# Performance work log

Measured on AMD Instinct MI355X. Metric: run time of the kernel, lower is better.

Reference implementation:

```python
import jax, jax.numpy as jnp
import numpy as np

V, BS, L, H, D = 32000, 2048, 6, 12, 768
B, T = 2, 2048
HD = D // H  # 64
STD = 0.02


def _ln(x, w, b):
    m = x.mean(-1, keepdims=True)
    v = x.var(-1, keepdims=True)
    return (x - m) / jnp.sqrt(v + 1e-5) * w + b


def setup_inputs() -> dict:
    key = jax.random.key(0)
    ks = jax.random.split(key, 7)
    idx = jax.random.randint(ks[0], (B, T), 0, V)
    tok_emb = jax.random.normal(ks[1], (V, D), jnp.float32) * STD   # tied with lm_head
    pos_emb = jax.random.normal(ks[2], (BS, D), jnp.float32) * STD
    qkv_w = jax.random.normal(ks[3], (L, D, 3 * D), jnp.float32) * STD
    out_w = jax.random.normal(ks[4], (L, D, D), jnp.float32) * STD
    ff1_w = jax.random.normal(ks[5], (L, D, 4 * D), jnp.float32) * STD
    ff2_w = jax.random.normal(ks[6], (L, 4 * D, D), jnp.float32) * STD
    ln1_w = jnp.ones((L, D)); ln1_b = jnp.zeros((L, D))
    ln2_w = jnp.ones((L, D)); ln2_b = jnp.zeros((L, D))
    lnf_w = jnp.ones((D,));  lnf_b = jnp.zeros((D,))
    return dict(idx=idx, tok_emb=tok_emb, pos_emb=pos_emb,
                ln1_w=ln1_w, ln1_b=ln1_b, qkv_w=qkv_w, out_w=out_w,
                ln2_w=ln2_w, ln2_b=ln2_b, ff1_w=ff1_w, ff2_w=ff2_w,
                lnf_w=lnf_w, lnf_b=lnf_b)


def reference(idx, tok_emb, pos_emb, ln1_w, ln1_b, qkv_w, out_w,
              ln2_w, ln2_b, ff1_w, ff2_w, lnf_w, lnf_b):
    Bb, Tt = idx.shape
    x = tok_emb[idx] + pos_emb[:Tt]          # [B,T,D]
    mask = jnp.tril(jnp.ones((Tt, Tt), bool))  # causal
    scale = jnp.asarray(np.sqrt(HD), x.dtype)

    def layer(x, p):
        l1w, l1b, Wqkv, Wout, l2w, l2b, W1, W2 = p
        h = _ln(x, l1w, l1b)
        q, k, v = jnp.split(h @ Wqkv, 3, axis=-1)
        hd = lambda t: t.reshape(Bb, Tt, H, HD).transpose(0, 2, 1, 3)  # [B,H,T,hd]
        q, k, v = hd(q), hd(k), hd(v)
        att = jnp.einsum('bhqd,bhkd->bhqk', q, k) / scale
        att = jnp.where(mask, att, -jnp.inf)
        att = jax.nn.softmax(att, axis=-1)
        y = jnp.einsum('bhqk,bhkd->bhqd', att, v)
        y = y.transpose(0, 2, 1, 3).reshape(Bb, Tt, D)
        x = x + y @ Wout
        h2 = _ln(x, l2w, l2b)
        x = x + jax.nn.gelu(h2 @ W1, approximate=False) @ W2
        return x, None

    x, _ = jax.lax.scan(layer, x, (ln1_w, ln1_b, qkv_w, out_w, ln2_w, ln2_b, ff1_w, ff2_w))
    x = _ln(x, lnf_w, lnf_b)
    return x @ tok_emb.T  # tied lm_head -> [B,T,V]
```

## Files before the change

### kernel.cpp

```cpp
#include <hip/hip_runtime.h>
#include <hip/hip_bf16.h>
#include <math.h>

typedef short short8 __attribute__((ext_vector_type(8)));
typedef short short4v __attribute__((ext_vector_type(4)));
typedef float f32x4 __attribute__((ext_vector_type(4)));
typedef unsigned short ushort_t;
typedef unsigned int uint_t;

#define D_MODEL 768
#define L_LAYERS 6
#define N_TOK 4096
#define T_SEQ 2048
#define H_HEADS 12
#define V_VOCAB 32000
#define L2E 1.44269504088896340736f

__device__ __forceinline__ ushort_t f2b(float f) {
  uint_t u = __builtin_bit_cast(uint_t, f);
  u += 0x7fffu + ((u >> 16) & 1u);
  return (ushort_t)(u >> 16);
}

__device__ __forceinline__ void gload_lds16(const void* g, void* l) {
  __builtin_amdgcn_global_load_lds(
      (const __attribute__((address_space(1))) unsigned int*)g,
      (__attribute__((address_space(3))) unsigned int*)l, 16, 0, 0);
}

__global__ void embed_kernel(const int* __restrict__ idx, const float* __restrict__ tok,
                             const float* __restrict__ pos, float* __restrict__ x) {
  int n = blockIdx.x;
  int tok_id = idx[n];
  int t = n & (T_SEQ - 1);
  const float* tr = tok + (size_t)tok_id * D_MODEL;
  const float* pr = pos + (size_t)t * D_MODEL;
  float* xr = x + (size_t)n * D_MODEL;
  for (int k = threadIdx.x; k < D_MODEL; k += 256) xr[k] = tr[k] + pr[k];
}

__global__ void ln_kernel(const float* __restrict__ x, const float* __restrict__ w,
                          const float* __restrict__ b, ushort_t* __restrict__ out) {
  int r = blockIdx.x, tid = threadIdx.x;
  const float* xr = x + (size_t)r * D_MODEL;
  float v0 = xr[tid], v1 = xr[tid + 256], v2 = xr[tid + 512];
  __shared__ float red[8];
  int l = tid & 63, wv = tid >> 6;
  float s = v0 + v1 + v2;
#pragma unroll
  for (int m = 32; m >= 1; m >>= 1) s += __shfl_xor(s, m, 64);
  if (l == 0) red[wv] = s;
  __syncthreads();
  float mean = (red[0] + red[1] + red[2] + red[3]) * (1.f / 768.f);
  float t0 = v0 - mean, t1 = v1 - mean, t2 = v2 - mean;
  float sq = t0 * t0 + t1 * t1 + t2 * t2;
#pragma unroll
  for (int m = 32; m >= 1; m >>= 1) sq += __shfl_xor(sq, m, 64);
  if (l == 0) red[4 + wv] = sq;
  __syncthreads();
  float var = (red[4] + red[5] + red[6] + red[7]) * (1.f / 768.f);
  float rstd = rsqrtf(var + 1e-5f);
  ushort_t* orow = out + (size_t)r * D_MODEL;
  orow[tid]       = f2b(t0 * rstd * w[tid] + b[tid]);
  orow[tid + 256] = f2b(t1 * rstd * w[tid + 256] + b[tid + 256]);
  orow[tid + 512] = f2b(t2 * rstd * w[tid + 512] + b[tid + 512]);
}

__global__ void transpose_cast_kernel(const float* __restrict__ in, ushort_t* __restrict__ out,
                                      int R, int C) {
  __shared__ float tile[32][33];
  size_t zoff = (size_t)blockIdx.z * R * C;
  in += zoff; out += zoff;
  int c0 = blockIdx.x * 32, r0 = blockIdx.y * 32;
  int tx = threadIdx.x, ty = threadIdx.y;
#pragma unroll
  for (int i = 0; i < 4; i++)
    tile[ty + i * 8][tx] = in[(size_t)(r0 + ty + i * 8) * C + (c0 + tx)];
  __syncthreads();
#pragma unroll
  for (int i = 0; i < 4; i++)
    out[(size_t)(c0 + ty + i * 8) * R + (r0 + tx)] = f2b(tile[tx][ty + i * 8]);
}

__global__ void cast_kernel(const float* __restrict__ in, ushort_t* __restrict__ out, int n) {
  for (int i = blockIdx.x * 256 + threadIdx.x; i < n; i += gridDim.x * 256)
    out[i] = f2b(in[i]);
}

#define EPI_STORE 0
#define EPI_ADD 1
#define EPI_GELU 2
#define EPI_CASTB 3

template <int EPI>
__global__ __launch_bounds__(256) void gemm_nt(const ushort_t* __restrict__ A,
                                               const ushort_t* __restrict__ B,
                                               float* __restrict__ Cf,
                                               ushort_t* __restrict__ Cb,
                                               int M, int N, int K) {
  __shared__ __align__(16) ushort_t As[128 * 32];
  __shared__ __align__(16) ushort_t Bs[128 * 32];
  int t = threadIdx.x;
  int l = t & 63, wv = t >> 6;
  int wm = (wv >> 1) * 64, wn = (wv & 1) * 64;

  int nwg = gridDim.x * gridDim.y;
  int bid = blockIdx.y * gridDim.x + blockIdx.x;
  int qn = nwg >> 3, r8 = nwg & 7;
  int xcd = bid & 7, pos = bid >> 3;
  int wg = (xcd < r8 ? xcd * (qn + 1) : r8 * (qn + 1) + (xcd - r8) * qn) + pos;
  int bn = wg % gridDim.x, bm = wg / gridDim.x;

  int fr = l & 15, fq = l >> 4;

  int srow = t >> 2;
  int scol = (t & 3) * 8;
  const ushort_t* gA = A + (size_t)(bm * 128 + srow) * K + scol;
  const ushort_t* gB = B + (size_t)(bn * 128 + srow) * K + scol;
  ushort_t* lA0 = &As[(wv * 16) * 32];
  ushort_t* lA1 = &As[(64 + wv * 16) * 32];
  ushort_t* lB0 = &Bs[(wv * 16) * 32];
  ushort_t* lB1 = &Bs[(64 + wv * 16) * 32];

  f32x4 acc[4][4];
#pragma unroll
  for (int i = 0; i < 4; i++)
#pragma unroll
    for (int j = 0; j < 4; j++) acc[i][j] = (f32x4){0.f, 0.f, 0.f, 0.f};

  for (int kt = 0; kt < K; kt += 32) {
    gload_lds16(gA + kt, lA0);
    gload_lds16(gA + (size_t)64 * K + kt, lA1);
    gload_lds16(gB + kt, lB0);
    gload_lds16(gB + (size_t)64 * K + kt, lB1);
    __syncthreads();
    short8 af[4], bf[4];
#pragma unroll
    for (int i = 0; i < 4; i++)
      af[i] = *(const short8*)&As[(wm + i * 16 + fr) * 32 + fq * 8];
#pragma unroll
    for (int j = 0; j < 4; j++)
      bf[j] = *(const short8*)&Bs[(wn + j * 16 + fr) * 32 + fq * 8];
#pragma unroll
    for (int i = 0; i < 4; i++)
#pragma unroll
      for (int j = 0; j < 4; j++)
        acc[i][j] = __builtin_amdgcn_mfma_f32_16x16x32_bf16(af[i], bf[j], acc[i][j], 0, 0, 0);
    __syncthreads();
  }

  int row0 = bm * 128 + wm + fq * 4;
  int col0 = bn * 128 + wn + fr;
#pragma unroll
  for (int i = 0; i < 4; i++) {
#pragma unroll
    for (int j = 0; j < 4; j++) {
#pragma unroll
      for (int r = 0; r < 4; r++) {
        int row = row0 + i * 16 + r;
        int col = col0 + j * 16;
        size_t off = (size_t)row * N + col;
        float v = acc[i][j][r];
        if (EPI == EPI_STORE) {
          Cf[off] = v;
        } else if (EPI == EPI_ADD) {
          Cf[off] += v;
        } else if (EPI == EPI_GELU) {
          Cb[off] = f2b(0.5f * v * (1.f + erff(v * 0.70710678118f)));
        } else {
          Cb[off] = f2b(v);
        }
      }
    }
  }
}

__global__ __launch_bounds__(256) void attn_mfma(const ushort_t* __restrict__ qkv,
                                                 ushort_t* __restrict__ y) {
  __shared__ __align__(16) ushort_t Ks[64 * 64];
  __shared__ __align__(16) ushort_t Vt[64 * 64];

  int id = blockIdx.x;
  int bh = id % 24;
  int qb = 31 - id / 24;
  int b = bh / H_HEADS, h = bh % H_HEADS;
  int t = threadIdx.x, l = t & 63, w = t >> 6;
  int ql = l & 15, kg = l >> 4;
  int q0 = qb * 64;
  size_t base = (size_t)b * T_SEQ * 2304;
  int qrow = q0 + w * 16 + ql;

  const ushort_t* qptr = qkv + base + (size_t)qrow * 2304 + h * 64 + kg * 8;
  short8 qf0 = *(const short8*)qptr;
  short8 qf1 = *(const short8*)(qptr + 32);

  float mrun = -INFINITY, lrun = 0.f;
  f32x4 o[4];
#pragma unroll
  for (int jd = 0; jd < 4; jd++) o[jd] = (f32x4){0.f, 0.f, 0.f, 0.f};

  const ushort_t* kbase = qkv + base + 768 + h * 64;
  const ushort_t* vbase = qkv + base + 1536 + h * 64;

  for (int kt = 0; kt <= q0; kt += 64) {
#pragma unroll
    for (int i = 0; i < 2; i++) {
      int c = i * 256 + t;
      int key = c >> 3, dc = c & 7;
      short8 k8 = *(const short8*)(kbase + (size_t)(kt + key) * 2304 + dc * 8);
      *(short8*)&Ks[key * 64 + ((dc ^ (key & 7)) * 8)] = k8;
      int vd0 = dc * 8;
      short8 v8 = *(const short8*)(vbase + (size_t)(kt + key) * 2304 + vd0);
#pragma unroll
      for (int e = 0; e < 8; e++) {
        int d = vd0 + e;
        Vt[d * 64 + (((key >> 3) ^ (d & 7)) * 8) + (key & 7)] = (ushort_t)v8[e];
      }
    }
    __syncthreads();

    f32x4 s[4];
#pragma unroll
    for (int kb = 0; kb < 4; kb++) {
      s[kb] = (f32x4){0.f, 0.f, 0.f, 0.f};
      short8 kfa = *(const short8*)&Ks[(kb * 16 + ql) * 64 + ((kg ^ (ql & 7)) * 8)];
      s[kb] = __builtin_amdgcn_mfma_f32_16x16x32_bf16(kfa, qf0, s[kb], 0, 0, 0);
      short8 kfb = *(const short8*)&Ks[(kb * 16 + ql) * 64 + (((kg + 4) ^ (ql & 7)) * 8)];
      s[kb] = __builtin_amdgcn_mfma_f32_16x16x32_bf16(kfb, qf1, s[kb], 0, 0, 0);
    }
#pragma unroll
    for (int kb = 0; kb < 4; kb++)
#pragma unroll
      for (int r = 0; r < 4; r++) s[kb][r] *= 0.125f;

    if (kt == q0) {
      int qloc = w * 16 + ql;
#pragma unroll
      for (int kb = 0; kb < 4; kb++)
#pragma unroll
        for (int r = 0; r < 4; r++) {
          int keyloc = kb * 16 + kg * 4 + r;
          if (keyloc > qloc) s[kb][r] = -INFINITY;
        }
    }

    float pm = -INFINITY;
#pragma unroll
    for (int kb = 0; kb < 4; kb++)
#pragma unroll
      for (int r = 0; r < 4; r++) pm = fmaxf(pm, s[kb][r]);
    pm = fmaxf(pm, __shfl_xor(pm, 16, 64));
    pm = fmaxf(pm, __shfl_xor(pm, 32, 64));
    float mnew = fmaxf(mrun, pm);
    float ps = 0.f;
#pragma unroll
    for (int kb = 0; kb < 4; kb++)
#pragma unroll
      for (int r = 0; r < 4; r++) {
        float p = exp2f((s[kb][r] - mnew) * L2E);
        s[kb][r] = p;
        ps += p;
      }
    ps += __shfl_xor(ps, 16, 64);
    ps += __shfl_xor(ps, 32, 64);
    float alpha = exp2f((mrun - mnew) * L2E);
    lrun = lrun * alpha + ps;
    mrun = mnew;
#pragma unroll
    for (int jd = 0; jd < 4; jd++)
#pragma unroll
      for (int r = 0; r < 4; r++) o[jd][r] *= alpha;

#pragma unroll
    for (int h2 = 0; h2 < 2; h2++) {
      short8 pb;
#pragma unroll
      for (int e = 0; e < 8; e++) {
        int r = e & 3, eb = e >> 2;
        int src = ql + 16 * (2 * (kg & 1) + eb);
        float vA = __shfl(s[2 * h2][r], src, 64);
        float vB = __shfl(s[2 * h2 + 1][r], src, 64);
        float v = (kg >> 1) ? vB : vA;
        pb[e] = (short)f2b(v);
      }
#pragma unroll
      for (int jd = 0; jd < 4; jd++) {
        short8 vf = *(const short8*)&Vt[(jd * 16 + ql) * 64 + (((kg + 4 * h2) ^ (ql & 7)) * 8)];
        o[jd] = __builtin_amdgcn_mfma_f32_16x16x32_bf16(vf, pb, o[jd], 0, 0, 0);
      }
    }
    __syncthreads();
  }

  float inv = 1.f / lrun;
  size_t yb = (size_t)(b * T_SEQ + qrow) * D_MODEL + h * 64;
#pragma unroll
  for (int jd = 0; jd < 4; jd++) {
    short4v pk;
#pragma unroll
    for (int r = 0; r < 4; r++) pk[r] = (short)f2b(o[jd][r] * inv);
    *(short4v*)&y[yb + jd * 16 + kg * 4] = pk;
  }
}

extern "C" void kernel_launch(void* const* d_in, const int* in_sizes, int n_in,
                              void* d_out, int out_size, void* d_ws, size_t ws_size,
                              hipStream_t stream) {
  const int*   idx     = (const int*)d_in[0];
  const float* tok_emb = (const float*)d_in[1];
  const float* pos_emb = (const float*)d_in[2];
  const float* ln1_w   = (const float*)d_in[3];
  const float* ln1_b   = (const float*)d_in[4];
  const float* qkv_w   = (const float*)d_in[5];
  const float* out_w   = (const float*)d_in[6];
  const float* ln2_w   = (const float*)d_in[7];
  const float* ln2_b   = (const float*)d_in[8];
  const float* ff1_w   = (const float*)d_in[9];
  const float* ff2_w   = (const float*)d_in[10];
  const float* lnf_w   = (const float*)d_in[11];
  const float* lnf_b   = (const float*)d_in[12];
  float* out = (float*)d_out;

  char* ws = (char*)d_ws;
  ushort_t* WqkvT = (ushort_t*)ws; ws += (size_t)L_LAYERS * 2304 * 768 * 2;
  ushort_t* WoutT = (ushort_t*)ws; ws += (size_t)L_LAYERS * 768 * 768 * 2;
  ushort_t* W1T   = (ushort_t*)ws; ws += (size_t)L_LAYERS * 3072 * 768 * 2;
  ushort_t* W2T   = (ushort_t*)ws; ws += (size_t)L_LAYERS * 768 * 3072 * 2;
  ushort_t* EmbB  = (ushort_t*)ws; ws += (size_t)V_VOCAB * 768 * 2;
  float*    x     = (float*)ws;    ws += (size_t)N_TOK * 768 * 4;
  ushort_t* hbuf  = (ushort_t*)ws; ws += (size_t)N_TOK * 768 * 2;
  ushort_t* qkvb  = (ushort_t*)ws; ws += (size_t)N_TOK * 2304 * 2;
  ushort_t* ybuf  = (ushort_t*)ws; ws += (size_t)N_TOK * 768 * 2;
  ushort_t* abuf  = (ushort_t*)ws; ws += (size_t)N_TOK * 3072 * 2;

  dim3 tb(32, 8);
  transpose_cast_kernel<<<dim3(2304 / 32, 768 / 32, 6), tb, 0, stream>>>(qkv_w, WqkvT, 768, 2304);
  transpose_cast_kernel<<<dim3(768 / 32, 768 / 32, 6), tb, 0, stream>>>(out_w, WoutT, 768, 768);
  transpose_cast_kernel<<<dim3(3072 / 32, 768 / 32, 6), tb, 0, stream>>>(ff1_w, W1T, 768, 3072);
  transpose_cast_kernel<<<dim3(768 / 32, 3072 / 32, 6), tb, 0, stream>>>(ff2_w, W2T, 3072, 768);
  cast_kernel<<<12000, 256, 0, stream>>>(tok_emb, EmbB, V_VOCAB * 768);
  embed_kernel<<<N_TOK, 256, 0, stream>>>(idx, tok_emb, pos_emb, x);

  for (int layer = 0; layer < L_LAYERS; layer++) {
    ln_kernel<<<N_TOK, 256, 0, stream>>>(x, ln1_w + layer * 768, ln1_b + layer * 768, hbuf);
    gemm_nt<EPI_CASTB><<<dim3(2304 / 128, N_TOK / 128), 256, 0, stream>>>(
        hbuf, WqkvT + (size_t)layer * 2304 * 768, nullptr, qkvb, N_TOK, 2304, 768);
    attn_mfma<<<24 * 32, 256, 0, stream>>>(qkvb, ybuf);
    gemm_nt<EPI_ADD><<<dim3(768 / 128, N_TOK / 128), 256, 0, stream>>>(
        ybuf, WoutT + (size_t)layer * 768 * 768, x, nullptr, N_TOK, 768, 768);
    ln_kernel<<<N_TOK, 256, 0, stream>>>(x, ln2_w + layer * 768, ln2_b + layer * 768, hbuf);
    gemm_nt<EPI_GELU><<<dim3(3072 / 128, N_TOK / 128), 256, 0, stream>>>(
        hbuf, W1T + (size_t)layer * 3072 * 768, nullptr, abuf, N_TOK, 3072, 768);
    gemm_nt<EPI_ADD><<<dim3(768 / 128, N_TOK / 128), 256, 0, stream>>>(
        abuf, W2T + (size_t)layer * 768 * 3072, x, nullptr, N_TOK, 768, 3072);
  }
  ln_kernel<<<N_TOK, 256, 0, stream>>>(x, lnf_w, lnf_b, hbuf);
  gemm_nt<EPI_STORE><<<dim3(V_VOCAB / 128, N_TOK / 128), 256, 0, stream>>>(
      hbuf, EmbB, out, nullptr, N_TOK, V_VOCAB, 768);
}
```

Before: 2.660 ms.

## Add triple-buffered 256-row GEMM with XCD-aware tile mapping for large GEMMs

Introduces a new 512-thread GEMM kernel with 256xBN tiles, a three-stage LDS ring buffer fed by direct global-to-LDS loads, XOR-swizzled LDS layout, and s_setprio around the MFMA blocks. Workgroup IDs are remapped so consecutive tiles land on the same XCD, for better L2 reuse. The QKV, FF1 and LM-head GEMMs use it, aiming to hide global load latency behind MFMA work and raise per-block reuse. Larger tiles mean fewer blocks for the smaller GEMMs, and the hand-placed waitcnt/barrier scheme depends on an exact count of loads in flight.

```diff
diff --git a/kernel.cpp b/kernel.cpp
--- a/kernel.cpp
+++ b/kernel.cpp
@@ -153,6 +153,144 @@
   int col0 = bn * 128 + wn + fr;
 #pragma unroll
   for (int i = 0; i < 4; i++) {
+#pragma unroll
+    for (int j = 0; j < 4; j++) {
+#pragma unroll
+      for (int r = 0; r < 4; r++) {
+        int row = row0 + i * 16 + r;
+        int col = col0 + j * 16;
+        size_t off = (size_t)row * N + col;
+        float v = acc[i][j][r];
+        if (EPI == EPI_STORE) {
+          Cf[off] = v;
+        } else if (EPI == EPI_ADD) {
+          Cf[off] += v;
+        } else if (EPI == EPI_GELU) {
+          Cb[off] = f2b(0.5f * v * (1.f + erff(v * 0.70710678118f)));
+        } else {
+          Cb[off] = f2b(v);
+        }
+      }
+    }
+  }
+}
+
+template <int BN, int EPI>
+__global__ __launch_bounds__(512) void gemm_nt_pipe(const ushort_t* __restrict__ A,
+                                                    const ushort_t* __restrict__ B,
+                                                    float* __restrict__ Cf,
+                                                    ushort_t* __restrict__ Cb,
+                                                    int M, int N, int K) {
+  constexpr int WGM = (BN == 256) ? 2 : 4;
+  constexpr int WGN = 8 / WGM;
+  constexpr int WTM = 256 / WGM;
+  constexpr int NI = WTM / 16;
+  constexpr int NLB = (BN == 256) ? 2 : 1;
+  __shared__ __align__(16) ushort_t As[3][256 * 32];
+  __shared__ __align__(16) ushort_t Bs[3][BN * 32];
+
+  int t = threadIdx.x, l = t & 63, wid = t >> 6;
+  int fr = l & 15, fq = l >> 4;
+  int wm_g = wid / WGN, wn_g = wid % WGN;
+  int RM = wm_g * WTM, CN = wn_g * 64;
+
+  int nbm = M >> 8;
+  int nwg = gridDim.x;
+  int bid = blockIdx.x;
+  int q8 = nwg >> 3, r8 = nwg & 7;
+  int xcd = bid & 7, pos = bid >> 3;
+  int wg = (xcd < r8 ? xcd * (q8 + 1) : r8 * (q8 + 1) + (xcd - r8) * q8) + pos;
+  int bm = wg % nbm, bn = wg / nbm;
+
+  int rlow = l >> 2;
+  int rowA0 = (wid * 2) * 16 + rlow;
+  int rowA1 = (wid * 2 + 1) * 16 + rlow;
+  const ushort_t* gA0 = A + (size_t)(bm * 256 + rowA0) * K + (((l & 3) ^ ((rowA0 >> 1) & 3)) * 8);
+  const ushort_t* gA1 = A + (size_t)(bm * 256 + rowA1) * K + (((l & 3) ^ ((rowA1 >> 1) & 3)) * 8);
+  int rowB0 = (wid * NLB) * 16 + rlow;
+  int rowB1 = (wid * NLB + 1) * 16 + rlow;
+  const ushort_t* gB0 = B + (size_t)(bn * BN + rowB0) * K + (((l & 3) ^ ((rowB0 >> 1) & 3)) * 8);
+  const ushort_t* gB1 = B + (size_t)(bn * BN + rowB1) * K + (((l & 3) ^ ((rowB1 >> 1) & 3)) * 8);
+
+  f32x4 acc[NI][4];
+#pragma unroll
+  for (int i = 0; i < NI; i++)
+#pragma unroll
+    for (int j = 0; j < 4; j++) acc[i][j] = (f32x4){0.f, 0.f, 0.f, 0.f};
+
+  int nt = K >> 5;
+
+#pragma unroll
+  for (int s = 0; s < 2; s++) {
+    gload_lds16(gA0 + s * 32, &As[s][(wid * 2) * 512]);
+    gload_lds16(gA1 + s * 32, &As[s][(wid * 2 + 1) * 512]);
+    gload_lds16(gB0 + s * 32, &Bs[s][(wid * NLB) * 512]);
+    if constexpr (NLB == 2) gload_lds16(gB1 + s * 32, &Bs[s][(wid * 2 + 1) * 512]);
+  }
+  if constexpr (NLB == 2) asm volatile("s_waitcnt vmcnt(4)" ::: "memory");
+  else                    asm volatile("s_waitcnt vmcnt(3)" ::: "memory");
+  __builtin_amdgcn_s_barrier();
+  __builtin_amdgcn_sched_barrier(0);
+
+  int cur = 0, nxt = 2;
+  for (int kt = 0; kt < nt; kt++) {
+    int ts = (kt + 2 < nt) ? kt + 2 : nt - 1;
+    int ko = ts * 32;
+    gload_lds16(gA0 + ko, &As[nxt][(wid * 2) * 512]);
+    gload_lds16(gA1 + ko, &As[nxt][(wid * 2 + 1) * 512]);
+
+    short8 bfr[4];
+#pragma unroll
+    for (int j = 0; j < 4; j++) {
+      int rr = CN + j * 16 + fr;
+      bfr[j] = *(const short8*)&Bs[cur][rr * 32 + ((fq ^ ((rr >> 1) & 3)) * 8)];
+    }
+    short8 afr[4];
+#pragma unroll
+    for (int i = 0; i < 4; i++) {
+      int rr = RM + i * 16 + fr;
+      afr[i] = *(const short8*)&As[cur][rr * 32 + ((fq ^ ((rr >> 1) & 3)) * 8)];
+    }
+    if constexpr (NLB == 1) gload_lds16(gB0 + ko, &Bs[nxt][(wid * NLB) * 512]);
+
+    __builtin_amdgcn_s_setprio(1);
+#pragma unroll
+    for (int i = 0; i < 4; i++)
+#pragma unroll
+      for (int j = 0; j < 4; j++)
+        acc[i][j] = __builtin_amdgcn_mfma_f32_16x16x32_bf16(afr[i], bfr[j], acc[i][j], 0, 0, 0);
+    __builtin_amdgcn_s_setprio(0);
+
+    if constexpr (BN == 256) {
+      gload_lds16(gB0 + ko, &Bs[nxt][(wid * 2) * 512]);
+      gload_lds16(gB1 + ko, &Bs[nxt][(wid * 2 + 1) * 512]);
+      short8 af2[4];
+#pragma unroll
+      for (int i = 0; i < 4; i++) {
+        int rr = RM + (4 + i) * 16 + fr;
+        af2[i] = *(const short8*)&As[cur][rr * 32 + ((fq ^ ((rr >> 1) & 3)) * 8)];
+      }
+      __builtin_amdgcn_s_setprio(1);
+#pragma unroll
+      for (int i = 0; i < 4; i++)
+#pragma unroll
+        for (int j = 0; j < 4; j++)
+          acc[4 + i][j] = __builtin_amdgcn_mfma_f32_16x16x32_bf16(af2[i], bfr[j], acc[4 + i][j], 0, 0, 0);
+      __builtin_amdgcn_s_setprio(0);
+    }
+
+    if constexpr (NLB == 2) asm volatile("s_waitcnt vmcnt(4)" ::: "memory");
+    else                    asm volatile("s_waitcnt vmcnt(3)" ::: "memory");
+    __builtin_amdgcn_s_barrier();
+    __builtin_amdgcn_sched_barrier(0);
+    cur = (cur + 1 == 3) ? 0 : cur + 1;
+    nxt = (nxt + 1 == 3) ? 0 : nxt + 1;
+  }
+
+  int row0 = bm * 256 + RM + fq * 4;
+  int col0 = bn * BN + CN + fr;
+#pragma unroll
+  for (int i = 0; i < NI; i++) {
 #pragma unroll
     for (int j = 0; j < 4; j++) {
 #pragma unroll
@@ -343,18 +481,18 @@
 
   for (int layer = 0; layer < L_LAYERS; layer++) {
     ln_kernel<<<N_TOK, 256, 0, stream>>>(x, ln1_w + layer * 768, ln1_b + layer * 768, hbuf);
-    gemm_nt<EPI_CASTB><<<dim3(2304 / 128, N_TOK / 128), 256, 0, stream>>>(
+    gemm_nt_pipe<128, EPI_CASTB><<<(2304 / 128) * (N_TOK / 256), 512, 0, stream>>>(
         hbuf, WqkvT + (size_t)layer * 2304 * 768, nullptr, qkvb, N_TOK, 2304, 768);
     attn_mfma<<<24 * 32, 256, 0, stream>>>(qkvb, ybuf);
     gemm_nt<EPI_ADD><<<dim3(768 / 128, N_TOK / 128), 256, 0, stream>>>(
         ybuf, WoutT + (size_t)layer * 768 * 768, x, nullptr, N_TOK, 768, 768);
     ln_kernel<<<N_TOK, 256, 0, stream>>>(x, ln2_w + layer * 768, ln2_b + layer * 768, hbuf);
-    gemm_nt<EPI_GELU><<<dim3(3072 / 128, N_TOK / 128), 256, 0, stream>>>(
+    gemm_nt_pipe<128, EPI_GELU><<<(3072 / 128) * (N_TOK / 256), 512, 0, stream>>>(
         hbuf, W1T + (size_t)layer * 3072 * 768, nullptr, abuf, N_TOK, 3072, 768);
     gemm_nt<EPI_ADD><<<dim3(768 / 128, N_TOK / 128), 256, 0, stream>>>(
         abuf, W2T + (size_t)layer * 768 * 3072, x, nullptr, N_TOK, 768, 3072);
   }
   ln_kernel<<<N_TOK, 256, 0, stream>>>(x, lnf_w, lnf_b, hbuf);
-  gemm_nt<EPI_STORE><<<dim3(V_VOCAB / 128, N_TOK / 128), 256, 0, stream>>>(
+  gemm_nt_pipe<256, EPI_STORE><<<(V_VOCAB / 256) * (N_TOK / 256), 512, 0, stream>>>(
       hbuf, EmbB, out, nullptr, N_TOK, V_VOCAB, 768);
 }
```

Measured after the change: 2.676 ms. Within noise of the previous version (+0.6%).
